# Performance work log

Hardware: AMD Instinct MI355X
Metric: run time of the kernel (lower is better)

The kernel has to match this reference:

```python
import jax, jax.numpy as jnp
import numpy as np

N, C_IN, C_OUT, T, V, S = 128, 64, 64, 128, 25, 3
R = C_IN // 8  # rel_channels = in_channels // rel_reduction
BN_EPS = 1e-5


def setup_inputs() -> dict:
    key = jax.random.key(0)
    ks = jax.random.split(key, 12)
    sd = lambda fan: 1.0 / np.sqrt(fan)
    return {
        "x": jax.random.normal(ks[0], (N, C_IN, T, V), dtype=jnp.float32),
        # per-subset CTRGC 1x1-conv weights (stacked over the S subsets)
        "W1": jax.random.normal(ks[1], (S, R, C_IN), dtype=jnp.float32) * sd(C_IN),
        "b1": jnp.zeros((S, R), dtype=jnp.float32),
        "W2": jax.random.normal(ks[2], (S, R, C_IN), dtype=jnp.float32) * sd(C_IN),
        "b2": jnp.zeros((S, R), dtype=jnp.float32),
        "W3": jax.random.normal(ks[3], (S, C_OUT, C_IN), dtype=jnp.float32) * sd(C_IN),
        "b3": jnp.zeros((S, C_OUT), dtype=jnp.float32),
        "W4": jax.random.normal(ks[4], (S, C_OUT, R), dtype=jnp.float32) * sd(R),
        "b4": jnp.zeros((S, C_OUT), dtype=jnp.float32),
        # adaptive adjacency PA [S, V, V] and per-subset alpha
        "PA": jax.random.uniform(ks[5], (S, V, V), dtype=jnp.float32) * (1.0 / V),
        "alpha": jnp.ones((S,), dtype=jnp.float32),
        # BatchNorm2d affine params (bn_init scale 1e-5 in the original)
        "bn_weight": jnp.full((C_OUT,), 1e-5, dtype=jnp.float32),
        "bn_bias": jnp.zeros((C_OUT,), dtype=jnp.float32),
    }


def _ctrgc(x, W1, b1, W2, b2, W3, b3, W4, b4, A_i, alpha_i):
    # x: [N, C, T, V]
    t = x.shape[2]
    # conv1(x).mean(-2): 1x1 conv then mean over T -> [N, R, V]
    x1 = jnp.einsum('nctv,rc->nrv', x, W1) / t + b1[None, :, None]
    x2 = jnp.einsum('nctv,rc->nrv', x, W2) / t + b2[None, :, None]
    # conv3(x): [N, Cout, T, V]
    x3 = jnp.einsum('nctv,oc->notv', x, W3) + b3[None, :, None, None]
    # tanh(x1[..., u, None] - x2[..., None, v]) -> [N, R, V, V]
    d = jnp.tanh(x1[:, :, :, None] - x2[:, :, None, :])
    # conv4 (1x1 over the VxV map): [N, Cout, V, V]
    adj = jnp.einsum('nruv,or->nouv', d, W4) + b4[None, :, None, None]
    adj = adj * alpha_i + A_i[None, None, :, :]
    # einsum 'ncuv,nctv->nctu'
    return jnp.einsum('nouv,notv->notu', adj, x3)


def reference(x, W1, b1, W2, b2, W3, b3, W4, b4, PA, alpha, bn_weight, bn_bias):
    y = None
    for i in range(PA.shape[0]):  # num_subset = 3 structurally distinct branches
        z = _ctrgc(x, W1[i], b1[i], W2[i], b2[i], W3[i], b3[i], W4[i], b4[i],
                   PA[i], alpha[i])
        y = z if y is None else y + z
    # BatchNorm2d, training mode (batch statistics over N, T, V per channel)
    mean = y.mean(axis=(0, 2, 3), keepdims=True)
    var = ((y - mean) ** 2).mean(axis=(0, 2, 3), keepdims=True)
    y = (y - mean) * jax.lax.rsqrt(var + BN_EPS) * bn_weight[None, :, None, None] \
        + bn_bias[None, :, None, None]
    y = y + x  # residual (in_channels == out_channels -> identity)
    return jax.nn.relu(y)
```

## Files before the change

kernel.cpp:

```cpp
#include <hip/hip_runtime.h>
#include <hip/hip_bf16.h>


typedef __attribute__((ext_vector_type(4))) float f32x4;
typedef __attribute__((ext_vector_type(2))) float f32x2;
typedef long long i64;

#define ADJ8_OFF  0
#define W3F8_OFF  25165824
#define XT8_OFF   25178112
#define Y8_OFF    51392512
#define XBAR_OFF  77606912
#define PART_OFF  78426112
#define COEF_OFF  78491648

__device__ inline unsigned short f2bf(float f) {
    union { float f; unsigned int u; } x; x.f = f;
    unsigned int u = x.u;
    return (unsigned short)((u + 0x7FFFu + ((u >> 16) & 1u)) >> 16);
}

__global__ void k_zero(float* xbar) {
    int i = blockIdx.x * 256 + threadIdx.x;
    if (i < 204800) xbar[i] = 0.f;
}

__global__ void k_w3prep(const float* __restrict__ W3, unsigned char* __restrict__ w3f) {
    int g = blockIdx.x * 512 + threadIdx.x;
    if (g >= 1536) return;
    int grp = g >> 6, lane = g & 63;
    int s = grp >> 3, kb = (grp >> 2) & 1, ot = grp & 3;
    int o = ot * 16 + (lane & 15);
    int c0 = kb * 32 + (lane >> 4) * 8;
    const float* src = W3 + (s * 64 + o) * 64 + c0;
    unsigned int p0 = __builtin_amdgcn_cvt_pk_fp8_f32(src[0], src[1], 0, false);
    p0 = __builtin_amdgcn_cvt_pk_fp8_f32(src[2], src[3], p0, true);
    unsigned int p1 = __builtin_amdgcn_cvt_pk_fp8_f32(src[4], src[5], 0, false);
    p1 = __builtin_amdgcn_cvt_pk_fp8_f32(src[6], src[7], p1, true);
    *(uint2*)(w3f + (grp * 64 + lane) * 8) = make_uint2(p0, p1);
}

__launch_bounds__(512)
__global__ void k_prep(const float* __restrict__ x, float* __restrict__ xbar,
                       unsigned char* __restrict__ xT) {
    __shared__ unsigned short xl[64 * 404];
    int bid = blockIdx.x;
    int n = bid >> 3, tc = bid & 7;
    int tid = threadIdx.x;
    const float* xs = x + (size_t)n * 204800 + tc * 400;
    for (int idx = tid; idx < 6400; idx += 512) {
        int c = idx / 100, r4 = idx - c * 100;
        float4 q = *(const float4*)(xs + c * 3200 + r4 * 4);
        unsigned int lo = (unsigned int)f2bf(q.x) | ((unsigned int)f2bf(q.y) << 16);
        unsigned int hi = (unsigned int)f2bf(q.z) | ((unsigned int)f2bf(q.w) << 16);
        *(uint2*)(xl + c * 404 + r4 * 4) = make_uint2(lo, hi);
    }
    __syncthreads();
    for (int i = tid; i < 1600; i += 512) {
        int c = i / 25, v = i - c * 25;
        float ssum = 0.f;
#pragma unroll
        for (int t = 0; t < 16; t++) {
            unsigned int b = xl[c * 404 + t * 25 + v];
            union { unsigned int u; float f; } cv; cv.u = b << 16;
            ssum += cv.f;
        }
        atomicAdd(&xbar[n * 1600 + i], ssum * (1.f / 128.f));
    }
    unsigned int* out = (unsigned int*)(xT) + (size_t)n * 51200 + tc * 6400;
    for (int j = tid; j < 6400; j += 512) {
        int cq = j & 15, tv = j >> 4;
        float f[4];
#pragma unroll
        for (int e = 0; e < 4; e++) {
            unsigned int b = xl[(4 * cq + e) * 404 + tv];
            union { unsigned int u; float g; } cv; cv.u = b << 16;
            f[e] = cv.g;
        }
        unsigned int pk = __builtin_amdgcn_cvt_pk_fp8_f32(f[0], f[1], 0, false);
        pk = __builtin_amdgcn_cvt_pk_fp8_f32(f[2], f[3], pk, true);
        out[j] = pk;
    }
}

__global__ void k_adj(const float* __restrict__ xbar,
                      const float* __restrict__ W1, const float* __restrict__ b1,
                      const float* __restrict__ W2, const float* __restrict__ b2,
                      const float* __restrict__ W4, const float* __restrict__ b4,
                      const float* __restrict__ PA, const float* __restrict__ alpha,
                      unsigned char* __restrict__ adjf) {
    int sb = blockIdx.x;
    int s = sb >> 7, n = sb & 127;
    __shared__ float xb[1600], w1l[512], w2l[512], w4l[512], b4l[64], pal[625];
    __shared__ float x1l[200], x2l[200];
    __shared__ float dt[8][25][28];
    int tid = threadIdx.x;
    for (int i = tid; i < 1600; i += 256) xb[i] = xbar[n * 1600 + i];
    for (int i = tid; i < 512; i += 256) {
        w1l[i] = W1[s * 512 + i];
        w2l[i] = W2[s * 512 + i];
        w4l[i] = W4[s * 512 + i];
    }
    if (tid < 64) b4l[tid] = b4[s * 64 + tid];
    for (int i = tid; i < 625; i += 256) pal[i] = PA[s * 625 + i];
    __syncthreads();
    if (tid < 200) {
        int r = tid / 25, v = tid % 25;
        float a1 = b1[s * 8 + r], a2 = b2[s * 8 + r];
        for (int c = 0; c < 64; c++) {
            float xv = xb[c * 25 + v];
            a1 += w1l[r * 64 + c] * xv;
            a2 += w2l[r * 64 + c] * xv;
        }
        x1l[tid] = a1;
        x2l[tid] = a2;
    }
    __syncthreads();
    for (int i = tid; i < 5000; i += 256) {
        int r = i / 625, uv = i % 625, u = uv / 25, v = uv % 25;
        dt[r][u][v] = tanhf(x1l[r * 25 + u] - x2l[r * 25 + v]);
    }
    for (int i = tid; i < 600; i += 256) {
        int r = i / 75, rem = i % 75, u = rem / 3, v = 25 + rem % 3;
        dt[r][u][v] = 0.f;
    }
    __syncthreads();

    int f = tid * 4;
    int lane = (f >> 3) & 63;
    int j0 = f & 7;
    int u = ((f >> 9) << 4) + (lane & 15);
    int v0 = ((lane >> 4) << 3) + j0;
    bool uok = (u < 25);
    float4 dr[8];
    if (uok && v0 < 28) {
#pragma unroll
        for (int r = 0; r < 8; r++) dr[r] = *(const float4*)&dt[r][u][v0];
    } else {
#pragma unroll
        for (int r = 0; r < 8; r++) { dr[r].x = dr[r].y = dr[r].z = dr[r].w = 0.f; }
    }
    float al = alpha[s];
    bool vok[4]; float pae[4];
#pragma unroll
    for (int e = 0; e < 4; e++) {
        int v = v0 + e;
        vok[e] = uok && (v < 25);
        pae[e] = vok[e] ? pal[u * 25 + v] : 0.f;
    }
    unsigned char* outp = adjf + ((size_t)(s * 128 + n)) * 65536 + f;
    for (int o = 0; o < 64; o++) {
        float b4o = b4l[o];
        float acc[4];
#pragma unroll
        for (int e = 0; e < 4; e++) {
            acc[e] = 0.f;
            if (vok[e]) {
                float dot = b4o;
#pragma unroll
                for (int r = 0; r < 8; r++) {
                    float dv = (e == 0) ? dr[r].x : (e == 1) ? dr[r].y : (e == 2) ? dr[r].z : dr[r].w;
                    dot += w4l[o * 8 + r] * dv;
                }
                acc[e] = dot * al + pae[e];
            }
        }
        unsigned int pk = __builtin_amdgcn_cvt_pk_fp8_f32(acc[0], acc[1], 0, false);
        pk = __builtin_amdgcn_cvt_pk_fp8_f32(acc[2], acc[3], pk, true);
        *(unsigned int*)(outp + o * 1024) = pk;
    }
}

#define STAGE1(S, BUF) do {                                                              \
    const unsigned char* wp_ = w3f + ((S) * 8 + ot) * 512 + lane * 8;                    \
    i64 bw0_ = *(const i64*)(wp_);                                                       \
    i64 bw1_ = *(const i64*)(wp_ + 2048);                                                \
    float bias_ = b3l[(S) * 64 + ot * 16 + l15];                                         \
    _Pragma("unroll")                                                                    \
    for (int i_ = 0; i_ < 4; i_++) {                                                     \
        f32x4 d_ = __builtin_amdgcn_mfma_f32_16x16x32_fp8_fp8(af0[i_], bw0_, zero4, 0, 0, 0); \
        d_ = __builtin_amdgcn_mfma_f32_16x16x32_fp8_fp8(af1[i_], bw1_, d_, 0, 0, 0);     \
        int mf_ = w + 8 * i_;                                                            \
        unsigned int pk_ = __builtin_amdgcn_cvt_pk_fp8_f32(d_[0] + bias_, d_[1] + bias_, 0, false); \
        pk_ = __builtin_amdgcn_cvt_pk_fp8_f32(d_[2] + bias_, d_[3] + bias_, pk_, true);  \
        *(unsigned int*)(x3l[BUF] + l15 * 648 + (mf_ >> 1) * 40 + ((mf_ & 1) << 4) + l4 * 4) = pk_; \
    } } while (0)

#define STAGE2(S, BUF) do {                                                              \
    _Pragma("unroll")                                                                    \
    for (int oj_ = 0; oj_ < 2; oj_++) {                                                  \
        i64 a_ = *(const i64*)(x3l[BUF] + (2 * w + oj_) * 648 + l15 * 40 + l4 * 8);      \
        yacc[oj_ * 2 + 0] = __builtin_amdgcn_mfma_f32_16x16x32_fp8_fp8(a_, badj[(S) * 4 + oj_ * 2 + 0], yacc[oj_ * 2 + 0], 0, 0, 0); \
        yacc[oj_ * 2 + 1] = __builtin_amdgcn_mfma_f32_16x16x32_fp8_fp8(a_, badj[(S) * 4 + oj_ * 2 + 1], yacc[oj_ * 2 + 1], 0, 0, 0); \
    } } while (0)

__launch_bounds__(512, 4)
__global__ void k_main(const unsigned char* __restrict__ xT, const float* __restrict__ b3g,
                       const unsigned char* __restrict__ w3f,
                       const unsigned char* __restrict__ adjf,
                       unsigned char* __restrict__ y8, float* __restrict__ partials) {
    __shared__ unsigned char x3l[2][16 * 648];
    __shared__ unsigned char ylds[8][800];
    __shared__ float b3l[192];

    int bid = blockIdx.x;
    int n = bid & 127, ot = bid >> 7;
    int tid = threadIdx.x;
    int w = tid >> 6, lane = tid & 63, l15 = lane & 15, l4 = lane >> 4;
    int oa = ot * 16 + 2 * w;

    if (tid < 192) b3l[tid] = b3g[tid];

    i64 badj[12];
    {
        const unsigned char* ap = adjf + (size_t)n * 65536 + (size_t)oa * 1024 + lane * 8;
#pragma unroll
        for (int s = 0; s < 3; s++)
#pragma unroll
            for (int oj = 0; oj < 2; oj++)
#pragma unroll
                for (int ut = 0; ut < 2; ut++)
                    badj[s * 4 + oj * 2 + ut] =
                        *(const i64*)(ap + (size_t)s * 8388608 + oj * 1024 + ut * 512);
    }
    __syncthreads();

    f32x4 zero4 = {0.f, 0.f, 0.f, 0.f};
    float s1[2] = {0.f, 0.f}, s2[2] = {0.f, 0.f};
    const unsigned char* xTn = xT + (size_t)n * 204800;
    int vrow = ((w & 1) << 4) + l15;
    bool vok = vrow < 25;
    int vc = vok ? vrow : 24;

    for (int tc = 0; tc < 8; tc++) {
        i64 af0[4], af1[4];
#pragma unroll
        for (int i_ = 0; i_ < 4; i_++) {
            int mf_ = w + 8 * i_;
            int tvk = (mf_ >> 1) * 25 + vc;
            const unsigned char* p = xTn + (size_t)(tc * 400 + tvk) * 64 + l4 * 8;
            i64 a0 = *(const i64*)p;
            i64 a1 = *(const i64*)(p + 32);
            af0[i_] = vok ? a0 : 0;
            af1[i_] = vok ? a1 : 0;
        }
        f32x4 yacc[4] = {zero4, zero4, zero4, zero4};

        STAGE1(0, 0);
        __syncthreads();
        STAGE1(1, 1);
        STAGE2(0, 0);
        __syncthreads();
        STAGE1(2, 0);
        STAGE2(1, 1);
        __syncthreads();
        STAGE2(2, 0);

#pragma unroll
        for (int oj = 0; oj < 2; oj++) {
#pragma unroll
            for (int ut = 0; ut < 2; ut++) {
                f32x4 d = yacc[oj * 2 + ut];
                int u = ut * 16 + l15;
                s1[oj] += d[0] + d[1] + d[2] + d[3];
                s2[oj] += d[0] * d[0] + d[1] * d[1] + d[2] * d[2] + d[3] * d[3];
                if (u < 25) {
#pragma unroll
                    for (int r = 0; r < 4; r++) {
                        unsigned int b = __builtin_amdgcn_cvt_pk_fp8_f32(d[r], d[r], 0, false) & 0xFFu;
                        ylds[w][oj * 400 + (l4 * 4 + r) * 25 + u] = (unsigned char)b;
                    }
                }
            }
        }
        asm volatile("s_waitcnt lgkmcnt(0)" ::: "memory");
#pragma unroll
        for (int rep = 0; rep < 4; rep++) {
            int idx = lane + rep * 64;
            if (idx < 200) {
                int oj = idx >= 100 ? 1 : 0;
                size_t gb = ((size_t)(n * 64 + oa + oj) * 3200) + tc * 400 + (idx - oj * 100) * 4;
                *(unsigned int*)(y8 + gb) = *(const unsigned int*)(&ylds[w][idx * 4]);
            }
        }
        __syncthreads();
    }

#pragma unroll
    for (int oj = 0; oj < 2; oj++) {
        float a = s1[oj], b = s2[oj];
#pragma unroll
        for (int off = 1; off < 64; off <<= 1) {
            a += __shfl_xor(a, off);
            b += __shfl_xor(b, off);
        }
        if (lane == 0) {
            partials[((oa + oj) * 2 + 0) * 128 + n] = a;
            partials[((oa + oj) * 2 + 1) * 128 + n] = b;
        }
    }
}

__global__ void k_redcoef(const float* __restrict__ partials, const float* __restrict__ bnw,
                          const float* __restrict__ bnb, float* __restrict__ coef) {
    __shared__ float st[128];
    int tid = threadIdx.x;
    const float4* p = (const float4*)(partials + tid * 128);
    float a = 0.f;
#pragma unroll
    for (int i = 0; i < 32; i++) {
        float4 q = p[i];
        a += q.x + q.y + q.z + q.w;
    }
    st[tid] = a;
    __syncthreads();
    if (tid < 64) {
        const float inv = 1.f / 409600.f;
        float mean = st[2 * tid] * inv;
        float var = st[2 * tid + 1] * inv - mean * mean;
        float sc = bnw[tid] * rsqrtf(var + 1e-5f);
        coef[2 * tid] = sc;
        coef[2 * tid + 1] = bnb[tid] - mean * sc;
    }
}

__launch_bounds__(512)
__global__ void k_final(float* __restrict__ outp, const unsigned char* __restrict__ y8,
                        const float* __restrict__ x, const float* __restrict__ coef) {
    unsigned int i = blockIdx.x * 512u + threadIdx.x;
    unsigned int o = (i / 800u) & 63u;
    float sc = coef[o * 2], sh = coef[o * 2 + 1];
    unsigned int yw = ((const unsigned int*)y8)[i];
    f32x2 lo = __builtin_amdgcn_cvt_pk_f32_fp8(yw, false);
    f32x2 hi = __builtin_amdgcn_cvt_pk_f32_fp8(yw, true);
    float4 xv = ((const float4*)x)[i];
    float4 r;
    r.x = fmaxf(lo[0] * sc + sh + xv.x, 0.f);
    r.y = fmaxf(lo[1] * sc + sh + xv.y, 0.f);
    r.z = fmaxf(hi[0] * sc + sh + xv.z, 0.f);
    r.w = fmaxf(hi[1] * sc + sh + xv.w, 0.f);
    ((float4*)outp)[i] = r;
}

extern "C" void kernel_launch(void* const* d_in, const int* in_sizes, int n_in,
                              void* d_out, int out_size, void* d_ws, size_t ws_size,
                              hipStream_t stream) {
    const float* x    = (const float*)d_in[0];
    const float* W1   = (const float*)d_in[1];
    const float* b1   = (const float*)d_in[2];
    const float* W2   = (const float*)d_in[3];
    const float* b2   = (const float*)d_in[4];
    const float* W3   = (const float*)d_in[5];
    const float* b3   = (const float*)d_in[6];
    const float* W4   = (const float*)d_in[7];
    const float* b4   = (const float*)d_in[8];
    const float* PA   = (const float*)d_in[9];
    const float* alpha= (const float*)d_in[10];
    const float* bnw  = (const float*)d_in[11];
    const float* bnb  = (const float*)d_in[12];

    char* wsb = (char*)d_ws;
    unsigned char* adjf  = (unsigned char*)(wsb + ADJ8_OFF);
    unsigned char* w3f   = (unsigned char*)(wsb + W3F8_OFF);
    unsigned char* xT    = (unsigned char*)(wsb + XT8_OFF);
    unsigned char* y8    = (unsigned char*)(wsb + Y8_OFF);
    float* xbar     = (float*)(wsb + XBAR_OFF);
    float* partials = (float*)(wsb + PART_OFF);
    float* coef     = (float*)(wsb + COEF_OFF);
    float* outp     = (float*)d_out;

    hipLaunchKernelGGL(k_zero, dim3(800), dim3(256), 0, stream, xbar);
    hipLaunchKernelGGL(k_w3prep, dim3(3), dim3(512), 0, stream, W3, w3f);
    hipLaunchKernelGGL(k_prep, dim3(1024), dim3(512), 0, stream, x, xbar, xT);
    hipLaunchKernelGGL(k_adj, dim3(384), dim3(256), 0, stream,
                       xbar, W1, b1, W2, b2, W4, b4, PA, alpha, adjf);
    hipLaunchKernelGGL(k_main, dim3(512), dim3(512), 0, stream,
                       xT, b3, w3f, adjf, y8, partials);
    hipLaunchKernelGGL(k_redcoef, dim3(1), dim3(128), 0, stream, partials, bnw, bnb, coef);
    hipLaunchKernelGGL(k_final, dim3(12800), dim3(512), 0, stream, outp, y8, x, coef);
}
```

Before: 147.2 us.

## Split k_main time loop across two blocks and drop per-iteration barrier

Each k_main block now handles half of the T chunks, which doubles the grid to 1024 blocks so more work is in flight per CU. The occupancy hint in launch bounds rises from 4 to 6. The trailing __syncthreads at the end of each iteration is removed, and the shared x3 buffers alternate parity between iterations so no extra barrier is needed. BN partial sums are stored per half and the reduction kernel reads twice as many entries. The trade-off is that each block loads its adjacency fragments twice as often overall, and register pressure is tighter.

```diff
diff --git a/kernel.cpp b/kernel.cpp
--- a/kernel.cpp
+++ b/kernel.cpp
@@ -12,7 +12,7 @@
 #define Y8_OFF    51392512
 #define XBAR_OFF  77606912
 #define PART_OFF  78426112
-#define COEF_OFF  78491648
+#define COEF_OFF  78557184
 
 __device__ inline unsigned short f2bf(float f) {
     union { float f; unsigned int u; } x; x.f = f;
@@ -194,7 +194,7 @@
         yacc[oj_ * 2 + 1] = __builtin_amdgcn_mfma_f32_16x16x32_fp8_fp8(a_, badj[(S) * 4 + oj_ * 2 + 1], yacc[oj_ * 2 + 1], 0, 0, 0); \
     } } while (0)
 
-__launch_bounds__(512, 4)
+__launch_bounds__(512, 6)
 __global__ void k_main(const unsigned char* __restrict__ xT, const float* __restrict__ b3g,
                        const unsigned char* __restrict__ w3f,
                        const unsigned char* __restrict__ adjf,
@@ -204,7 +204,8 @@
     __shared__ float b3l[192];
 
     int bid = blockIdx.x;
-    int n = bid & 127, ot = bid >> 7;
+    int n = bid & 127, q = bid >> 7;
+    int ot = q >> 1, th = q & 1;
     int tid = threadIdx.x;
     int w = tid >> 6, lane = tid & 63, l15 = lane & 15, l4 = lane >> 4;
     int oa = ot * 16 + 2 * w;
@@ -232,29 +233,31 @@
     bool vok = vrow < 25;
     int vc = vok ? vrow : 24;
 
-    for (int tc = 0; tc < 8; tc++) {
+    for (int tc2 = 0; tc2 < 4; tc2++) {
+        int tc = th * 4 + tc2;
+        int p = tc2 & 1;
         i64 af0[4], af1[4];
 #pragma unroll
         for (int i_ = 0; i_ < 4; i_++) {
             int mf_ = w + 8 * i_;
             int tvk = (mf_ >> 1) * 25 + vc;
-            const unsigned char* p = xTn + (size_t)(tc * 400 + tvk) * 64 + l4 * 8;
-            i64 a0 = *(const i64*)p;
-            i64 a1 = *(const i64*)(p + 32);
+            const unsigned char* pp = xTn + (size_t)(tc * 400 + tvk) * 64 + l4 * 8;
+            i64 a0 = *(const i64*)pp;
+            i64 a1 = *(const i64*)(pp + 32);
             af0[i_] = vok ? a0 : 0;
             af1[i_] = vok ? a1 : 0;
         }
         f32x4 yacc[4] = {zero4, zero4, zero4, zero4};
 
-        STAGE1(0, 0);
+        STAGE1(0, p);
         __syncthreads();
-        STAGE1(1, 1);
-        STAGE2(0, 0);
+        STAGE1(1, p ^ 1);
+        STAGE2(0, p);
         __syncthreads();
-        STAGE1(2, 0);
-        STAGE2(1, 1);
+        STAGE1(2, p);
+        STAGE2(1, p ^ 1);
         __syncthreads();
-        STAGE2(2, 0);
+        STAGE2(2, p);
 
 #pragma unroll
         for (int oj = 0; oj < 2; oj++) {
@@ -283,7 +286,6 @@
                 *(unsigned int*)(y8 + gb) = *(const unsigned int*)(&ylds[w][idx * 4]);
             }
         }
-        __syncthreads();
     }
 
 #pragma unroll
@@ -295,8 +297,8 @@
             b += __shfl_xor(b, off);
         }
         if (lane == 0) {
-            partials[((oa + oj) * 2 + 0) * 128 + n] = a;
-            partials[((oa + oj) * 2 + 1) * 128 + n] = b;
+            partials[((oa + oj) * 2 + 0) * 256 + th * 128 + n] = a;
+            partials[((oa + oj) * 2 + 1) * 256 + th * 128 + n] = b;
         }
     }
 }
@@ -305,10 +307,10 @@
                           const float* __restrict__ bnb, float* __restrict__ coef) {
     __shared__ float st[128];
     int tid = threadIdx.x;
-    const float4* p = (const float4*)(partials + tid * 128);
+    const float4* p = (const float4*)(partials + tid * 256);
     float a = 0.f;
 #pragma unroll
-    for (int i = 0; i < 32; i++) {
+    for (int i = 0; i < 64; i++) {
         float4 q = p[i];
         a += q.x + q.y + q.z + q.w;
     }
@@ -374,7 +376,7 @@
     hipLaunchKernelGGL(k_prep, dim3(1024), dim3(512), 0, stream, x, xbar, xT);
     hipLaunchKernelGGL(k_adj, dim3(384), dim3(256), 0, stream,
                        xbar, W1, b1, W2, b2, W4, b4, PA, alpha, adjf);
-    hipLaunchKernelGGL(k_main, dim3(512), dim3(512), 0, stream,
+    hipLaunchKernelGGL(k_main, dim3(1024), dim3(512), 0, stream,
                        xT, b3, w3f, adjf, y8, partials);
     hipLaunchKernelGGL(k_redcoef, dim3(1), dim3(128), 0, stream, partials, bnw, bnb, coef);
     hipLaunchKernelGGL(k_final, dim3(12800), dim3(512), 0, stream, outp, y8, x, coef);
```

Result: slower. 239.5 us (+62.7%).

## Replace xbar atomics with per-chunk partials, widen k_adj, prefetch next A fragments

Applied to the files above, without the earlier changes.

Removes the xbar zeroing kernel by having k_prep write per-time-chunk partial means that k_adj sums, replacing the global atomics. k_adj now launches 512 threads and splits the 64 output channels between two thread halves. k_main unrolls its 8 time chunks and double-buffers the A fragments from xT, loading the next chunk's fragments during the current chunk's compute. It also ping-pongs the LDS buffer index, which drops one barrier. The cost is more registers in k_main and a larger partials workspace.

```diff
diff --git a/kernel.cpp b/kernel.cpp
--- a/kernel.cpp
+++ b/kernel.cpp
@@ -10,19 +10,14 @@
 #define W3F8_OFF  25165824
 #define XT8_OFF   25178112
 #define Y8_OFF    51392512
-#define XBAR_OFF  77606912
-#define PART_OFF  78426112
-#define COEF_OFF  78491648
+#define XBARP_OFF 77606912
+#define PART_OFF  84160512
+#define COEF_OFF  84226048
 
 __device__ inline unsigned short f2bf(float f) {
     union { float f; unsigned int u; } x; x.f = f;
     unsigned int u = x.u;
     return (unsigned short)((u + 0x7FFFu + ((u >> 16) & 1u)) >> 16);
-}
-
-__global__ void k_zero(float* xbar) {
-    int i = blockIdx.x * 256 + threadIdx.x;
-    if (i < 204800) xbar[i] = 0.f;
 }
 
 __global__ void k_w3prep(const float* __restrict__ W3, unsigned char* __restrict__ w3f) {
@@ -41,7 +36,7 @@
 }
 
 __launch_bounds__(512)
-__global__ void k_prep(const float* __restrict__ x, float* __restrict__ xbar,
+__global__ void k_prep(const float* __restrict__ x, float* __restrict__ xbarp,
                        unsigned char* __restrict__ xT) {
     __shared__ unsigned short xl[64 * 404];
     int bid = blockIdx.x;
@@ -65,7 +60,7 @@
             union { unsigned int u; float f; } cv; cv.u = b << 16;
             ssum += cv.f;
         }
-        atomicAdd(&xbar[n * 1600 + i], ssum * (1.f / 128.f));
+        xbarp[((size_t)tc * 128 + n) * 1600 + i] = ssum * (1.f / 128.f);
     }
     unsigned int* out = (unsigned int*)(xT) + (size_t)n * 51200 + tc * 6400;
     for (int j = tid; j < 6400; j += 512) {
@@ -83,7 +78,8 @@
     }
 }
 
-__global__ void k_adj(const float* __restrict__ xbar,
+__launch_bounds__(512)
+__global__ void k_adj(const float* __restrict__ xbarp,
                       const float* __restrict__ W1, const float* __restrict__ b1,
                       const float* __restrict__ W2, const float* __restrict__ b2,
                       const float* __restrict__ W4, const float* __restrict__ b4,
@@ -95,14 +91,19 @@
     __shared__ float x1l[200], x2l[200];
     __shared__ float dt[8][25][28];
     int tid = threadIdx.x;
-    for (int i = tid; i < 1600; i += 256) xb[i] = xbar[n * 1600 + i];
-    for (int i = tid; i < 512; i += 256) {
+    for (int i = tid; i < 1600; i += 512) {
+        float a = 0.f;
+#pragma unroll
+        for (int tc = 0; tc < 8; tc++) a += xbarp[((size_t)tc * 128 + n) * 1600 + i];
+        xb[i] = a;
+    }
+    for (int i = tid; i < 512; i += 512) {
         w1l[i] = W1[s * 512 + i];
         w2l[i] = W2[s * 512 + i];
         w4l[i] = W4[s * 512 + i];
     }
     if (tid < 64) b4l[tid] = b4[s * 64 + tid];
-    for (int i = tid; i < 625; i += 256) pal[i] = PA[s * 625 + i];
+    for (int i = tid; i < 625; i += 512) pal[i] = PA[s * 625 + i];
     __syncthreads();
     if (tid < 200) {
         int r = tid / 25, v = tid % 25;
@@ -116,17 +117,18 @@
         x2l[tid] = a2;
     }
     __syncthreads();
-    for (int i = tid; i < 5000; i += 256) {
+    for (int i = tid; i < 5000; i += 512) {
         int r = i / 625, uv = i % 625, u = uv / 25, v = uv % 25;
         dt[r][u][v] = tanhf(x1l[r * 25 + u] - x2l[r * 25 + v]);
     }
-    for (int i = tid; i < 600; i += 256) {
+    for (int i = tid; i < 600; i += 512) {
         int r = i / 75, rem = i % 75, u = rem / 3, v = 25 + rem % 3;
         dt[r][u][v] = 0.f;
     }
     __syncthreads();
 
-    int f = tid * 4;
+    int tq = tid >> 8;
+    int f = (tid & 255) * 4;
     int lane = (f >> 3) & 63;
     int j0 = f & 7;
     int u = ((f >> 9) << 4) + (lane & 15);
@@ -149,7 +151,8 @@
         pae[e] = vok[e] ? pal[u * 25 + v] : 0.f;
     }
     unsigned char* outp = adjf + ((size_t)(s * 128 + n)) * 65536 + f;
-    for (int o = 0; o < 64; o++) {
+    int o0 = tq * 32;
+    for (int o = o0; o < o0 + 32; o++) {
         float b4o = b4l[o];
         float acc[4];
 #pragma unroll
@@ -171,15 +174,27 @@
     }
 }
 
-#define STAGE1(S, BUF) do {                                                              \
+#define LOADAF(D0, D1, TC) do {                                                          \
+    _Pragma("unroll")                                                                    \
+    for (int i_ = 0; i_ < 4; i_++) {                                                     \
+        int mf_ = w + 8 * i_;                                                            \
+        int tvk_ = (mf_ >> 1) * 25 + vc;                                                 \
+        const unsigned char* pp_ = xTn + (size_t)((TC) * 400 + tvk_) * 64 + l4 * 8;      \
+        i64 a0_ = *(const i64*)pp_;                                                      \
+        i64 a1_ = *(const i64*)(pp_ + 32);                                               \
+        D0[i_] = vok ? a0_ : 0;                                                          \
+        D1[i_] = vok ? a1_ : 0;                                                          \
+    } } while (0)
+
+#define STAGE1(S, BUF, AF0, AF1) do {                                                    \
     const unsigned char* wp_ = w3f + ((S) * 8 + ot) * 512 + lane * 8;                    \
     i64 bw0_ = *(const i64*)(wp_);                                                       \
     i64 bw1_ = *(const i64*)(wp_ + 2048);                                                \
     float bias_ = b3l[(S) * 64 + ot * 16 + l15];                                         \
     _Pragma("unroll")                                                                    \
     for (int i_ = 0; i_ < 4; i_++) {                                                     \
-        f32x4 d_ = __builtin_amdgcn_mfma_f32_16x16x32_fp8_fp8(af0[i_], bw0_, zero4, 0, 0, 0); \
-        d_ = __builtin_amdgcn_mfma_f32_16x16x32_fp8_fp8(af1[i_], bw1_, d_, 0, 0, 0);     \
+        f32x4 d_ = __builtin_amdgcn_mfma_f32_16x16x32_fp8_fp8(AF0[i_], bw0_, zero4, 0, 0, 0); \
+        d_ = __builtin_amdgcn_mfma_f32_16x16x32_fp8_fp8(AF1[i_], bw1_, d_, 0, 0, 0);     \
         int mf_ = w + 8 * i_;                                                            \
         unsigned int pk_ = __builtin_amdgcn_cvt_pk_fp8_f32(d_[0] + bias_, d_[1] + bias_, 0, false); \
         pk_ = __builtin_amdgcn_cvt_pk_fp8_f32(d_[2] + bias_, d_[3] + bias_, pk_, true);  \
@@ -192,6 +207,47 @@
         i64 a_ = *(const i64*)(x3l[BUF] + (2 * w + oj_) * 648 + l15 * 40 + l4 * 8);      \
         yacc[oj_ * 2 + 0] = __builtin_amdgcn_mfma_f32_16x16x32_fp8_fp8(a_, badj[(S) * 4 + oj_ * 2 + 0], yacc[oj_ * 2 + 0], 0, 0, 0); \
         yacc[oj_ * 2 + 1] = __builtin_amdgcn_mfma_f32_16x16x32_fp8_fp8(a_, badj[(S) * 4 + oj_ * 2 + 1], yacc[oj_ * 2 + 1], 0, 0, 0); \
+    } } while (0)
+
+#define CHUNK(TC, AC0, AC1, AN0, AN1, P) do {                                            \
+    f32x4 yacc[4] = {zero4, zero4, zero4, zero4};                                        \
+    STAGE1(0, P, AC0, AC1);                                                              \
+    __syncthreads();                                                                     \
+    STAGE1(1, (P) ^ 1, AC0, AC1);                                                        \
+    STAGE2(0, P);                                                                        \
+    __syncthreads();                                                                     \
+    STAGE1(2, P, AC0, AC1);                                                              \
+    STAGE2(1, (P) ^ 1);                                                                  \
+    if ((TC) < 7) LOADAF(AN0, AN1, (TC) + 1);                                            \
+    __syncthreads();                                                                     \
+    STAGE2(2, P);                                                                        \
+        \
+    _Pragma("unroll")                                                                    \
+    for (int oj = 0; oj < 2; oj++) {                                                     \
+        _Pragma("unroll")                                                                \
+        for (int ut = 0; ut < 2; ut++) {                                                 \
+            f32x4 d = yacc[oj * 2 + ut];                                                 \
+            int u = ut * 16 + l15;                                                       \
+            s1[oj] += d[0] + d[1] + d[2] + d[3];                                         \
+            s2[oj] += d[0] * d[0] + d[1] * d[1] + d[2] * d[2] + d[3] * d[3];             \
+            if (u < 25) {                                                                \
+                _Pragma("unroll")                                                        \
+                for (int r = 0; r < 4; r++) {                                            \
+                    unsigned int b = __builtin_amdgcn_cvt_pk_fp8_f32(d[r], d[r], 0, false) & 0xFFu; \
+                    ylds[w][oj * 400 + (l4 * 4 + r) * 25 + u] = (unsigned char)b;        \
+                }                                                                        \
+            }                                                                            \
+        }                                                                                \
+    }                                                                                    \
+    asm volatile("s_waitcnt lgkmcnt(0)" ::: "memory");                                   \
+    _Pragma("unroll")                                                                    \
+    for (int rep = 0; rep < 4; rep++) {                                                  \
+        int idx = lane + rep * 64;                                                       \
+        if (idx < 200) {                                                                 \
+            int oj = idx >= 100 ? 1 : 0;                                                 \
+            size_t gb = ((size_t)(n * 64 + oa + oj) * 3200) + (TC) * 400 + (idx - oj * 100) * 4; \
+            *(unsigned int*)(y8 + gb) = *(const unsigned int*)(&ylds[w][idx * 4]);       \
+        }                                                                                \
     } } while (0)
 
 __launch_bounds__(512, 4)
@@ -223,7 +279,6 @@
                     badj[s * 4 + oj * 2 + ut] =
                         *(const i64*)(ap + (size_t)s * 8388608 + oj * 1024 + ut * 512);
     }
-    __syncthreads();
 
     f32x4 zero4 = {0.f, 0.f, 0.f, 0.f};
     float s1[2] = {0.f, 0.f}, s2[2] = {0.f, 0.f};
@@ -232,59 +287,18 @@
     bool vok = vrow < 25;
     int vc = vok ? vrow : 24;
 
-    for (int tc = 0; tc < 8; tc++) {
-        i64 af0[4], af1[4];
-#pragma unroll
-        for (int i_ = 0; i_ < 4; i_++) {
-            int mf_ = w + 8 * i_;
-            int tvk = (mf_ >> 1) * 25 + vc;
-            const unsigned char* p = xTn + (size_t)(tc * 400 + tvk) * 64 + l4 * 8;
-            i64 a0 = *(const i64*)p;
-            i64 a1 = *(const i64*)(p + 32);
-            af0[i_] = vok ? a0 : 0;
-            af1[i_] = vok ? a1 : 0;
-        }
-        f32x4 yacc[4] = {zero4, zero4, zero4, zero4};
-
-        STAGE1(0, 0);
-        __syncthreads();
-        STAGE1(1, 1);
-        STAGE2(0, 0);
-        __syncthreads();
-        STAGE1(2, 0);
-        STAGE2(1, 1);
-        __syncthreads();
-        STAGE2(2, 0);
-
-#pragma unroll
-        for (int oj = 0; oj < 2; oj++) {
-#pragma unroll
-            for (int ut = 0; ut < 2; ut++) {
-                f32x4 d = yacc[oj * 2 + ut];
-                int u = ut * 16 + l15;
-                s1[oj] += d[0] + d[1] + d[2] + d[3];
-                s2[oj] += d[0] * d[0] + d[1] * d[1] + d[2] * d[2] + d[3] * d[3];
-                if (u < 25) {
-#pragma unroll
-                    for (int r = 0; r < 4; r++) {
-                        unsigned int b = __builtin_amdgcn_cvt_pk_fp8_f32(d[r], d[r], 0, false) & 0xFFu;
-                        ylds[w][oj * 400 + (l4 * 4 + r) * 25 + u] = (unsigned char)b;
-                    }
-                }
-            }
-        }
-        asm volatile("s_waitcnt lgkmcnt(0)" ::: "memory");
-#pragma unroll
-        for (int rep = 0; rep < 4; rep++) {
-            int idx = lane + rep * 64;
-            if (idx < 200) {
-                int oj = idx >= 100 ? 1 : 0;
-                size_t gb = ((size_t)(n * 64 + oa + oj) * 3200) + tc * 400 + (idx - oj * 100) * 4;
-                *(unsigned int*)(y8 + gb) = *(const unsigned int*)(&ylds[w][idx * 4]);
-            }
-        }
-        __syncthreads();
-    }
+    i64 afA0[4], afA1[4], afB0[4], afB1[4];
+    LOADAF(afA0, afA1, 0);
+    __syncthreads();
+
+    CHUNK(0, afA0, afA1, afB0, afB1, 0);
+    CHUNK(1, afB0, afB1, afA0, afA1, 1);
+    CHUNK(2, afA0, afA1, afB0, afB1, 0);
+    CHUNK(3, afB0, afB1, afA0, afA1, 1);
+    CHUNK(4, afA0, afA1, afB0, afB1, 0);
+    CHUNK(5, afB0, afB1, afA0, afA1, 1);
+    CHUNK(6, afA0, afA1, afB0, afB1, 0);
+    CHUNK(7, afB0, afB1, afA0, afA1, 1);
 
 #pragma unroll
     for (int oj = 0; oj < 2; oj++) {
@@ -364,16 +378,15 @@
     unsigned char* w3f   = (unsigned char*)(wsb + W3F8_OFF);
     unsigned char* xT    = (unsigned char*)(wsb + XT8_OFF);
     unsigned char* y8    = (unsigned char*)(wsb + Y8_OFF);
-    float* xbar     = (float*)(wsb + XBAR_OFF);
+    float* xbarp    = (float*)(wsb + XBARP_OFF);
     float* partials = (float*)(wsb + PART_OFF);
     float* coef     = (float*)(wsb + COEF_OFF);
     float* outp     = (float*)d_out;
 
-    hipLaunchKernelGGL(k_zero, dim3(800), dim3(256), 0, stream, xbar);
     hipLaunchKernelGGL(k_w3prep, dim3(3), dim3(512), 0, stream, W3, w3f);
-    hipLaunchKernelGGL(k_prep, dim3(1024), dim3(512), 0, stream, x, xbar, xT);
-    hipLaunchKernelGGL(k_adj, dim3(384), dim3(256), 0, stream,
-                       xbar, W1, b1, W2, b2, W4, b4, PA, alpha, adjf);
+    hipLaunchKernelGGL(k_prep, dim3(1024), dim3(512), 0, stream, x, xbarp, xT);
+    hipLaunchKernelGGL(k_adj, dim3(384), dim3(512), 0, stream,
+                       xbarp, W1, b1, W2, b2, W4, b4, PA, alpha, adjf);
     hipLaunchKernelGGL(k_main, dim3(512), dim3(512), 0, stream,
                        xT, b3, w3f, adjf, y8, partials);
     hipLaunchKernelGGL(k_redcoef, dim3(1), dim3(128), 0, stream, partials, bnw, bnb, coef);
```

Result: slower. 174.4 us (+18.5%).
